# Kernel optimization log

Measured on AMD Instinct MI355X. Metric: run time of the kernel, lower is better.

The kernel has to match this reference:

```python
import jax, jax.numpy as jnp
import numpy as np

B, H, W, D = 1, 256, 256, 256
HEADS, DH = 8, 64
INNER = HEADS * DH


def setup_inputs() -> dict:
    key = jax.random.key(0)
    ks = jax.random.split(key, 6)
    s = 0.02  # init scale for weights
    return {
        "x": jax.random.normal(ks[0], (B, H, W, D), jnp.float32),
        "edges": jax.random.normal(ks[1], (B, H, H, D), jnp.float32),
        "mask": jnp.ones((B, H, W), jnp.bool_),
        "ln_g": jnp.ones((D,), jnp.float32),
        "ln_b": jnp.zeros((D,), jnp.float32),
        "Wq": jax.random.normal(ks[2], (D, INNER), jnp.float32) * s,
        "Wkv": jax.random.normal(ks[3], (D, 2 * INNER), jnp.float32) * s,
        "Wo": jax.random.normal(ks[4], (INNER, D), jnp.float32) * s,
        "bo": jnp.zeros((D,), jnp.float32),
        "Wg": jnp.zeros((D, INNER), jnp.float32),  # gating weight init 0
        "bg": jnp.ones((INNER,), jnp.float32),     # gating bias init 1
        "We": jax.random.normal(ks[5], (D, HEADS), jnp.float32) * s,
    }


def reference(x, edges, mask, ln_g, ln_b, Wq, Wkv, Wo, bo, Wg, bg, We):
    b, h, w, d = x.shape
    heads = We.shape[1]
    inner = Wq.shape[1]
    dh = inner // heads
    scale = dh ** -0.5

    # LayerNorm over last dim (eps=1e-5)
    mu = jnp.mean(x, axis=-1, keepdims=True)
    var = jnp.mean((x - mu) ** 2, axis=-1, keepdims=True)
    xn = (x - mu) * jax.lax.rsqrt(var + 1e-5) * ln_g + ln_b

    # pair bias from edges: (b, heads, i, j) with i=j=h
    bias = jnp.einsum('bijd,dh->bhij', edges, We)

    # row attention: tokens along h, batch over (b, w)
    xw = jnp.transpose(xn, (0, 2, 1, 3))              # (b, w, h, d)
    q = (xw @ Wq).reshape(b, w, h, heads, dh)
    kv = (xw @ Wkv).reshape(b, w, h, 2, heads, dh)
    k, v = kv[..., 0, :, :], kv[..., 1, :, :]

    # (b, w, heads, i, j)
    dots = jnp.einsum('bwihd,bwjhd->bwhij', q, k) * scale
    dots = dots + bias[:, None]                       # broadcast over w

    m = jnp.transpose(mask, (0, 2, 1))                # (b, w, h)
    pair_mask = m[:, :, None, :, None] & m[:, :, None, None, :]
    dots = jnp.where(pair_mask, dots, -jnp.finfo(dots.dtype).max)

    attn = jax.nn.softmax(dots, axis=-1)
    out = jnp.einsum('bwhij,bwjhd->bwihd', attn, v).reshape(b, w, h, inner)

    gates = xw @ Wg + bg
    out = (out * gates) @ Wo + bo                     # (b, w, h, d)
    out = jnp.transpose(out, (0, 2, 1, 3))            # (b, h, w, d)
    return out  # axial_attn_count == 1
```

## Files before the change

kernel.cpp:

```cpp
#include <hip/hip_runtime.h>
#include <hip/hip_bf16.h>
#include <stdint.h>

#define Hh     256
#define Ww     256
#define Dd     256
#define NHEADS 8
#define DH     64
#define INNER  512

typedef __attribute__((ext_vector_type(8))) short  bf16x8;
typedef __attribute__((ext_vector_type(4))) float  f32x4;

__device__ __forceinline__ unsigned short f2bfu(float f){
  __hip_bfloat16 h = __float2bfloat16(f);
  return *reinterpret_cast<unsigned short*>(&h);
}
__device__ __forceinline__ float bfu2f(unsigned short u){
  union { uint32_t i; float f; } a; a.i = ((uint32_t)u) << 16; return a.f;
}

__device__ __forceinline__ void async_cp16(unsigned short* lds_base_uniform,
                                           const unsigned short* g){
  __builtin_amdgcn_global_load_lds(
      (const __attribute__((address_space(1))) void*)g,
      (__attribute__((address_space(3))) void*)lds_base_uniform,
      16, 0, 0);
}

__global__ __launch_bounds__(256) void ln_kernel(const float* __restrict__ x,
        const float* __restrict__ lng, const float* __restrict__ lnb,
        unsigned short* __restrict__ xnb){
  int wv = threadIdx.x >> 6, l = threadIdx.x & 63;
  int row = blockIdx.x * 4 + wv;
  int h = row >> 8, w = row & 255;
  float4 v = *(const float4*)(x + (size_t)row * Dd + l * 4);
  float s1 = v.x + v.y + v.z + v.w;
  float s2 = v.x*v.x + v.y*v.y + v.z*v.z + v.w*v.w;
  #pragma unroll
  for (int off = 32; off; off >>= 1){
    s1 += __shfl_xor(s1, off, 64);
    s2 += __shfl_xor(s2, off, 64);
  }
  float mu  = s1 * (1.0f/256.0f);
  float var = s2 * (1.0f/256.0f) - mu*mu;
  float rs  = rsqrtf(var + 1e-5f);
  float4 g = *(const float4*)(lng + l*4);
  float4 b = *(const float4*)(lnb + l*4);
  union { unsigned short u[4]; uint2 v2; } pk;
  pk.u[0] = f2bfu((v.x - mu)*rs*g.x + b.x);
  pk.u[1] = f2bfu((v.y - mu)*rs*g.y + b.y);
  pk.u[2] = f2bfu((v.z - mu)*rs*g.z + b.z);
  pk.u[3] = f2bfu((v.w - mu)*rs*g.w + b.w);
  *(uint2*)(xnb + ((size_t)w * Hh + h) * Dd + l * 4) = pk.v2;
}

__global__ __launch_bounds__(256) void bias_kernel(const float* __restrict__ edges,
        const float* __restrict__ We, float* __restrict__ bias){
  const int t = threadIdx.x, wv = t >> 6, l = t & 63;
  float Wr[4][8];
  #pragma unroll
  for (int q = 0; q < 4; q++){
    float4 w0 = *(const float4*)(We + (l*4 + q) * 8);
    float4 w1 = *(const float4*)(We + (l*4 + q) * 8 + 4);
    Wr[q][0]=w0.x; Wr[q][1]=w0.y; Wr[q][2]=w0.z; Wr[q][3]=w0.w;
    Wr[q][4]=w1.x; Wr[q][5]=w1.y; Wr[q][6]=w1.z; Wr[q][7]=w1.w;
  }
  const int base = (blockIdx.x * 4 + wv) * 16;
  for (int i = 0; i < 16; i += 2){
    float4 eA = *(const float4*)(edges + (size_t)(base + i)     * 256 + l * 4);
    float4 eB = *(const float4*)(edges + (size_t)(base + i + 1) * 256 + l * 4);
    float aA[8], aB[8];
    #pragma unroll
    for (int h = 0; h < 8; h++){
      aA[h] = eA.x*Wr[0][h] + eA.y*Wr[1][h] + eA.z*Wr[2][h] + eA.w*Wr[3][h];
      aB[h] = eB.x*Wr[0][h] + eB.y*Wr[1][h] + eB.z*Wr[2][h] + eB.w*Wr[3][h];
    }
    #pragma unroll
    for (int h = 0; h < 8; h++){
      #pragma unroll
      for (int off = 1; off < 8; off <<= 1){
        aA[h] += __shfl_xor(aA[h], off, 64);
        aB[h] += __shfl_xor(aB[h], off, 64);
      }
    }
    float vA = (l&1) ? ((l&2) ? ((l&4)?aA[7]:aA[3]) : ((l&4)?aA[5]:aA[1]))
                     : ((l&2) ? ((l&4)?aA[6]:aA[2]) : ((l&4)?aA[4]:aA[0]));
    float vB = (l&1) ? ((l&2) ? ((l&4)?aB[7]:aB[3]) : ((l&4)?aB[5]:aB[1]))
                     : ((l&2) ? ((l&4)?aB[6]:aB[2]) : ((l&4)?aB[4]:aB[0]));
    #pragma unroll
    for (int off = 8; off < 64; off <<= 1){
      vA += __shfl_xor(vA, off, 64);
      vB += __shfl_xor(vB, off, 64);
    }
    if (l < 8)       bias[(size_t)l       * 65536 + base + i]     = vA;
    else if (l < 16) bias[(size_t)(l & 7) * 65536 + base + i + 1] = vB;
  }
}

__global__ __launch_bounds__(256) void transpose_w(const float* __restrict__ src,
        unsigned short* __restrict__ dst, int K, int N){
  __shared__ float ts[32][33];
  int n0 = blockIdx.x * 32, k0 = blockIdx.y * 32;
  int tx = threadIdx.x & 31, ty = threadIdx.x >> 5;
  #pragma unroll
  for (int i = 0; i < 32; i += 8)
    ts[ty + i][tx] = src[(size_t)(k0 + ty + i) * N + n0 + tx];
  __syncthreads();
  #pragma unroll
  for (int i = 0; i < 32; i += 8)
    dst[(size_t)(n0 + ty + i) * K + k0 + tx] = f2bfu(ts[tx][ty + i]);
}

__global__ __launch_bounds__(512, 2) void fused_qkvg_attn(
        const unsigned short* __restrict__ xnb,
        const unsigned short* __restrict__ WtA,
        const float* __restrict__ bias_all,
        const float* __restrict__ bg,
        unsigned short* __restrict__ ao){
  __shared__ unsigned short smem[68096];
  unsigned short* Sst = smem;
  unsigned short* Kl  = smem + 32768;
  unsigned short* Vl  = smem + 51200;
  const int t    = threadIdx.x;
  const int bid  = blockIdx.x;
  const int w    = bid & 255, head = bid >> 8;
  const int lane = t & 63, wv = t >> 6;
  const int lm   = lane & 15, quad = lane >> 4;
  const int row4 = t >> 2;
  const int cc   = (t & 3) ^ ((t >> 3) & 3);
  const int wvb  = wv * 512;
  const int xr   = (quad ^ ((lm >> 1) & 3)) * 8;

  const unsigned short* gA0 = xnb + ((size_t)(w * 256 + row4)) * 256 + cc * 8;
  const unsigned short* gA1 = gA0 + 128 * 256;
  const int nB0 = row4, nB1 = row4 + 128;
  const unsigned short* gB0 = WtA + ((size_t)((nB0 >> 6) * 512 + head * 64 + (nB0 & 63))) * 256 + cc * 8;
  const unsigned short* gB1 = WtA + ((size_t)((nB1 >> 6) * 512 + head * 64 + (nB1 & 63))) * 256 + cc * 8;

  f32x4 acc[2][16];
  #pragma unroll
  for (int s = 0; s < 2; s++)
    #pragma unroll
    for (int nt = 0; nt < 16; nt++) acc[s][nt] = (f32x4){0.f,0.f,0.f,0.f};

  {
    async_cp16(Sst + wvb,               gA0);
    async_cp16(Sst + 4096 + wvb,        gA1);
    async_cp16(Sst + 8192 + wvb,        gB0);
    async_cp16(Sst + 12288 + wvb,       gB1);
  }
  __syncthreads();
  for (int step = 0; step < 8; step++){
    const int cur = step & 1;
    if (step < 7){
      const int k0 = (step + 1) * 32;
      async_cp16(Sst + (cur^1)*16384 + wvb,         gA0 + k0);
      async_cp16(Sst + (cur^1)*16384 + 4096 + wvb,  gA1 + k0);
      async_cp16(Sst + (cur^1)*16384 + 8192 + wvb,  gB0 + k0);
      async_cp16(Sst + (cur^1)*16384 + 12288 + wvb, gB1 + k0);
    }
    bf16x8 a0 = *(const bf16x8*)&Sst[cur*16384 + (wv*32      + lm) * 32 + xr];
    bf16x8 a1 = *(const bf16x8*)&Sst[cur*16384 + (wv*32 + 16 + lm) * 32 + xr];
    #pragma unroll
    for (int h8 = 0; h8 < 2; h8++){
      bf16x8 b[8];
      #pragma unroll
      for (int i = 0; i < 8; i++)
        b[i] = *(const bf16x8*)&Sst[cur*16384 + 8192 + ((h8*8 + i)*16 + lm) * 32 + xr];
      #pragma unroll
      for (int i = 0; i < 8; i++){
        acc[0][h8*8+i] = __builtin_amdgcn_mfma_f32_16x16x32_bf16(a0, b[i], acc[0][h8*8+i], 0, 0, 0);
        acc[1][h8*8+i] = __builtin_amdgcn_mfma_f32_16x16x32_bf16(a1, b[i], acc[1][h8*8+i], 0, 0, 0);
      }
    }
    __syncthreads();
  }

  #pragma unroll
  for (int s = 0; s < 2; s++){
    #pragma unroll
    for (int nt = 4; nt < 8; nt++){
      int d = (nt - 4) * 16 + lm;
      #pragma unroll
      for (int r = 0; r < 4; r++){
        int key = wv*32 + s*16 + quad*4 + r;
        Kl[key * 72 + d] = f2bfu(acc[s][nt][r]);
      }
    }
    #pragma unroll
    for (int nt = 8; nt < 12; nt++){
      int d  = (nt - 8) * 16 + lm;
      int j0 = wv*32 + s*16 + quad*4;
      union { unsigned short u[4]; uint2 v2; } pk;
      #pragma unroll
      for (int r = 0; r < 4; r++) pk.u[r] = f2bfu(acc[s][nt][r]);
      *(uint2*)&Vl[d * 264 + j0] = pk.v2;
    }
  }
  __syncthreads();

  unsigned short* Qb = Sst + wv * 4096;
  unsigned short* Pb = Qb + 1152;
  const float* bias_h = bias_all + (size_t)head * 65536;
  float bgv[4];
  #pragma unroll
  for (int nt = 0; nt < 4; nt++) bgv[nt] = bg[head * 64 + nt*16 + lm];

  #pragma unroll
  for (int qt = 0; qt < 2; qt++){
    const int qb = wv*32 + qt*16;
    #pragma unroll
    for (int nt = 0; nt < 4; nt++)
      #pragma unroll
      for (int r = 0; r < 4; r++)
        Qb[(quad*4 + r) * 72 + nt*16 + lm] = f2bfu(acc[qt][nt][r]);
    f32x4 s2[16];
    #pragma unroll
    for (int nt2 = 0; nt2 < 16; nt2++) s2[nt2] = (f32x4){0.f,0.f,0.f,0.f};
    #pragma unroll
    for (int c = 0; c < 2; c++){
      bf16x8 qf = *(const bf16x8*)&Qb[lm * 72 + c*32 + quad*8];
      #pragma unroll
      for (int nt2 = 0; nt2 < 16; nt2++){
        bf16x8 kf = *(const bf16x8*)&Kl[(nt2*16 + lm) * 72 + c*32 + quad*8];
        s2[nt2] = __builtin_amdgcn_mfma_f32_16x16x32_bf16(qf, kf, s2[nt2], 0, 0, 0);
      }
    }
    float mx[4] = {-3.0e38f, -3.0e38f, -3.0e38f, -3.0e38f};
    #pragma unroll
    for (int nt2 = 0; nt2 < 16; nt2++)
      #pragma unroll
      for (int r = 0; r < 4; r++){
        float b = bias_h[(size_t)(qb + quad*4 + r) * 256 + nt2*16 + lm];
        s2[nt2][r] = s2[nt2][r] * 0.125f + b;
        mx[r] = fmaxf(mx[r], s2[nt2][r]);
      }
    #pragma unroll
    for (int r = 0; r < 4; r++){
      #pragma unroll
      for (int off = 1; off < 16; off <<= 1) mx[r] = fmaxf(mx[r], __shfl_xor(mx[r], off, 64));
    }
    float sum[4] = {0.f, 0.f, 0.f, 0.f};
    #pragma unroll
    for (int nt2 = 0; nt2 < 16; nt2++)
      #pragma unroll
      for (int r = 0; r < 4; r++){
        s2[nt2][r] = __expf(s2[nt2][r] - mx[r]);
        sum[r] += s2[nt2][r];
      }
    #pragma unroll
    for (int r = 0; r < 4; r++){
      #pragma unroll
      for (int off = 1; off < 16; off <<= 1) sum[r] += __shfl_xor(sum[r], off, 64);
      sum[r] = 1.0f / sum[r];
    }
    f32x4 o[4];
    #pragma unroll
    for (int nt = 0; nt < 4; nt++) o[nt] = (f32x4){0.f,0.f,0.f,0.f};
    #pragma unroll
    for (int kh = 0; kh < 2; kh++){
      #pragma unroll
      for (int nt2 = 0; nt2 < 8; nt2++)
        #pragma unroll
        for (int r = 0; r < 4; r++)
          Pb[(quad*4 + r) * 136 + nt2*16 + lm] = f2bfu(s2[kh*8 + nt2][r] * sum[r]);
      #pragma unroll
      for (int c2 = 0; c2 < 4; c2++){
        bf16x8 pf = *(const bf16x8*)&Pb[lm * 136 + c2*32 + quad*8];
        #pragma unroll
        for (int nt = 0; nt < 4; nt++){
          bf16x8 vf = *(const bf16x8*)&Vl[(nt*16 + lm) * 264 + kh*128 + c2*32 + quad*8];
          o[nt] = __builtin_amdgcn_mfma_f32_16x16x32_bf16(pf, vf, o[nt], 0, 0, 0);
        }
      }
    }
    #pragma unroll
    for (int nt = 0; nt < 4; nt++)
      #pragma unroll
      for (int r = 0; r < 4; r++){
        float g = acc[qt][12 + nt][r] + bgv[nt];
        Qb[(quad*4 + r) * 72 + nt*16 + lm] = f2bfu(o[nt][r] * g);
      }
    int rr = lane >> 2, d0 = (lane & 3) * 16;
    bf16x8 o0 = *(const bf16x8*)&Qb[rr * 72 + d0];
    bf16x8 o1 = *(const bf16x8*)&Qb[rr * 72 + d0 + 8];
    size_t tok = (size_t)(w * 256 + qb + rr);
    *(bf16x8*)(ao + tok * INNER + head * DH + d0)     = o0;
    *(bf16x8*)(ao + tok * INNER + head * DH + d0 + 8) = o1;
  }
}

__global__ __launch_bounds__(256) void gemm_proj_tiled(
        const unsigned short* __restrict__ ao,
        const unsigned short* __restrict__ WtO,
        const float* __restrict__ bo,
        float* __restrict__ out){
  __shared__ unsigned short lds[2][10240];
  const int t    = threadIdx.x;
  const int m0   = blockIdx.x * 64;
  const int lane = t & 63, wv = t >> 6;
  const int lm   = lane & 15, quad = lane >> 4;
  const int row4 = t >> 2;
  const int cc   = (t & 3) ^ ((t >> 3) & 3);
  const int wvb  = wv * 512;
  const unsigned short* gA = ao + (size_t)(m0 + row4) * INNER + cc * 8;
  const unsigned short* gB[4];
  #pragma unroll
  for (int i = 0; i < 4; i++)
    gB[i] = WtO + (size_t)(i * 64 + row4) * INNER + cc * 8;
  const int xr = (quad ^ ((lm >> 1) & 3)) * 8;

  f32x4 acc[4][4];
  #pragma unroll
  for (int mt = 0; mt < 4; mt++)
    #pragma unroll
    for (int nt = 0; nt < 4; nt++) acc[mt][nt] = (f32x4){0.f,0.f,0.f,0.f};

  async_cp16(&lds[0][wvb], gA);
  #pragma unroll
  for (int i = 0; i < 4; i++)
    async_cp16(&lds[0][2048 + i * 2048 + wvb], gB[i]);
  __syncthreads();

  for (int step = 0; step < 16; step++){
    const int cur = step & 1;
    if (step < 15){
      const int k0 = (step + 1) * 32;
      async_cp16(&lds[cur ^ 1][wvb], gA + k0);
      #pragma unroll
      for (int i = 0; i < 4; i++)
        async_cp16(&lds[cur ^ 1][2048 + i * 2048 + wvb], gB[i] + k0);
    }
    bf16x8 a[4], b[4];
    #pragma unroll
    for (int mt = 0; mt < 4; mt++)
      a[mt] = *(const bf16x8*)&lds[cur][(mt * 16 + lm) * 32 + xr];
    #pragma unroll
    for (int nt = 0; nt < 4; nt++)
      b[nt] = *(const bf16x8*)&lds[cur][2048 + (wv * 64 + nt * 16 + lm) * 32 + xr];
    #pragma unroll
    for (int mt = 0; mt < 4; mt++)
      #pragma unroll
      for (int nt = 0; nt < 4; nt++)
        acc[mt][nt] = __builtin_amdgcn_mfma_f32_16x16x32_bf16(a[mt], b[nt], acc[mt][nt], 0, 0, 0);
    __syncthreads();
  }

  #pragma unroll
  for (int mt = 0; mt < 4; mt++)
    #pragma unroll
    for (int nt = 0; nt < 4; nt++){
      int col = wv * 64 + nt * 16 + lm;
      float bb = bo[col];
      #pragma unroll
      for (int r = 0; r < 4; r++){
        int row = m0 + mt * 16 + quad * 4 + r;
        int h = row & 255, ww = row >> 8;
        out[((size_t)h * Ww + ww) * Dd + col] = acc[mt][nt][r] + bb;
      }
    }
}

extern "C" void kernel_launch(void* const* d_in, const int* in_sizes, int n_in,
                              void* d_out, int out_size, void* d_ws, size_t ws_size,
                              hipStream_t stream){
  const float* x     = (const float*)d_in[0];
  const float* edges = (const float*)d_in[1];
  const float* ln_g  = (const float*)d_in[3];
  const float* ln_b  = (const float*)d_in[4];
  const float* Wq    = (const float*)d_in[5];
  const float* Wkv   = (const float*)d_in[6];
  const float* Wo    = (const float*)d_in[7];
  const float* bo    = (const float*)d_in[8];
  const float* Wg    = (const float*)d_in[9];
  const float* bg    = (const float*)d_in[10];
  const float* We    = (const float*)d_in[11];
  float* out = (float*)d_out;

  char* ws = (char*)d_ws;
  unsigned short* ao  = (unsigned short*)(ws + 33554432);
  unsigned short* WtO = (unsigned short*)(ws + 100663296);
  char* dob = (char*)d_out;
  unsigned short* xnb  = (unsigned short*)dob;
  float*          bias = (float*)(dob + 33554432);
  unsigned short* WtA  = (unsigned short*)(dob + 35651584);

  ln_kernel  <<<16384, 256, 0, stream>>>(x, ln_g, ln_b, xnb);
  bias_kernel<<< 1024, 256, 0, stream>>>(edges, We, bias);
  transpose_w<<<dim3(16,  8), 256, 0, stream>>>(Wq,  WtA,                     Dd, 512);
  transpose_w<<<dim3(32,  8), 256, 0, stream>>>(Wkv, WtA + (size_t)512*Dd,    Dd, 1024);
  transpose_w<<<dim3(16,  8), 256, 0, stream>>>(Wg,  WtA + (size_t)1536*Dd,   Dd, 512);
  transpose_w<<<dim3( 8, 16), 256, 0, stream>>>(Wo,  WtO,                     INNER, 256);
  fused_qkvg_attn<<<2048, 512, 0, stream>>>(xnb, WtA, bias, bg, ao);
  gemm_proj_tiled<<<1024, 256, 0, stream>>>(ao, WtO, bo, out);
}
```

Baseline: 461.8 us.

## Swizzle LDS layouts and transpose MFMA operands for vectorized Q/K/V/P stores

Swaps MFMA operand order for the Q and K projection tiles so each lane holds four consecutive columns, which allows packed 8-byte LDS stores. Padded LDS strides are replaced with XOR-swizzled layouts to avoid bank conflicts. The two query sub-tiles are processed together so each K/V fragment load feeds two MFMAs, and bias loads become float4 reads. Holding more accumulators live raises register pressure, which could cost occupancy or cause spills.

```diff
diff --git a/kernel.cpp b/kernel.cpp
--- a/kernel.cpp
+++ b/kernel.cpp
@@ -18,6 +18,11 @@
 }
 __device__ __forceinline__ float bfu2f(unsigned short u){
   union { uint32_t i; float f; } a; a.i = ((uint32_t)u) << 16; return a.f;
+}
+__device__ __forceinline__ uint2 pk4(f32x4 v){
+  union { unsigned short u[4]; uint2 d; } p;
+  p.u[0] = f2bfu(v[0]); p.u[1] = f2bfu(v[1]); p.u[2] = f2bfu(v[2]); p.u[3] = f2bfu(v[3]);
+  return p.d;
 }
 
 __device__ __forceinline__ void async_cp16(unsigned short* lds_base_uniform,
@@ -118,19 +123,19 @@
         const float* __restrict__ bias_all,
         const float* __restrict__ bg,
         unsigned short* __restrict__ ao){
-  __shared__ unsigned short smem[68096];
+  __shared__ unsigned short smem[65536];
   unsigned short* Sst = smem;
   unsigned short* Kl  = smem + 32768;
-  unsigned short* Vl  = smem + 51200;
+  unsigned short* Vl  = smem + 49152;
   const int t    = threadIdx.x;
-  const int bid  = blockIdx.x;
-  const int w    = bid & 255, head = bid >> 8;
+  const int w    = blockIdx.x & 255, head = blockIdx.x >> 8;
   const int lane = t & 63, wv = t >> 6;
   const int lm   = lane & 15, quad = lane >> 4;
   const int row4 = t >> 2;
   const int cc   = (t & 3) ^ ((t >> 3) & 3);
   const int wvb  = wv * 512;
   const int xr   = (quad ^ ((lm >> 1) & 3)) * 8;
+  const int sw8  = (lm & 7) << 3;
 
   const unsigned short* gA0 = xnb + ((size_t)(w * 256 + row4)) * 256 + cc * 8;
   const unsigned short* gA1 = gA0 + 128 * 256;
@@ -144,12 +149,10 @@
     #pragma unroll
     for (int nt = 0; nt < 16; nt++) acc[s][nt] = (f32x4){0.f,0.f,0.f,0.f};
 
-  {
-    async_cp16(Sst + wvb,               gA0);
-    async_cp16(Sst + 4096 + wvb,        gA1);
-    async_cp16(Sst + 8192 + wvb,        gB0);
-    async_cp16(Sst + 12288 + wvb,       gB1);
-  }
+  async_cp16(Sst + wvb,          gA0);
+  async_cp16(Sst + 4096 + wvb,   gA1);
+  async_cp16(Sst + 8192 + wvb,   gB0);
+  async_cp16(Sst + 12288 + wvb,  gB1);
   __syncthreads();
   for (int step = 0; step < 8; step++){
     const int cur = step & 1;
@@ -162,132 +165,144 @@
     }
     bf16x8 a0 = *(const bf16x8*)&Sst[cur*16384 + (wv*32      + lm) * 32 + xr];
     bf16x8 a1 = *(const bf16x8*)&Sst[cur*16384 + (wv*32 + 16 + lm) * 32 + xr];
-    #pragma unroll
-    for (int h8 = 0; h8 < 2; h8++){
+    {
       bf16x8 b[8];
       #pragma unroll
       for (int i = 0; i < 8; i++)
-        b[i] = *(const bf16x8*)&Sst[cur*16384 + 8192 + ((h8*8 + i)*16 + lm) * 32 + xr];
+        b[i] = *(const bf16x8*)&Sst[cur*16384 + 8192 + (i*16 + lm) * 32 + xr];
       #pragma unroll
       for (int i = 0; i < 8; i++){
-        acc[0][h8*8+i] = __builtin_amdgcn_mfma_f32_16x16x32_bf16(a0, b[i], acc[0][h8*8+i], 0, 0, 0);
-        acc[1][h8*8+i] = __builtin_amdgcn_mfma_f32_16x16x32_bf16(a1, b[i], acc[1][h8*8+i], 0, 0, 0);
+        acc[0][i] = __builtin_amdgcn_mfma_f32_16x16x32_bf16(b[i], a0, acc[0][i], 0, 0, 0);
+        acc[1][i] = __builtin_amdgcn_mfma_f32_16x16x32_bf16(b[i], a1, acc[1][i], 0, 0, 0);
+      }
+    }
+    {
+      bf16x8 b[8];
+      #pragma unroll
+      for (int i = 0; i < 8; i++)
+        b[i] = *(const bf16x8*)&Sst[cur*16384 + 8192 + ((8+i)*16 + lm) * 32 + xr];
+      #pragma unroll
+      for (int i = 0; i < 8; i++){
+        acc[0][8+i] = __builtin_amdgcn_mfma_f32_16x16x32_bf16(a0, b[i], acc[0][8+i], 0, 0, 0);
+        acc[1][8+i] = __builtin_amdgcn_mfma_f32_16x16x32_bf16(a1, b[i], acc[1][8+i], 0, 0, 0);
       }
     }
     __syncthreads();
   }
 
+  unsigned short* slot = Sst + wv * 4096;
   #pragma unroll
   for (int s = 0; s < 2; s++){
-    #pragma unroll
-    for (int nt = 4; nt < 8; nt++){
-      int d = (nt - 4) * 16 + lm;
-      #pragma unroll
-      for (int r = 0; r < 4; r++){
-        int key = wv*32 + s*16 + quad*4 + r;
-        Kl[key * 72 + d] = f2bfu(acc[s][nt][r]);
-      }
-    }
-    #pragma unroll
-    for (int nt = 8; nt < 12; nt++){
-      int d  = (nt - 8) * 16 + lm;
-      int j0 = wv*32 + s*16 + quad*4;
-      union { unsigned short u[4]; uint2 v2; } pk;
-      #pragma unroll
-      for (int r = 0; r < 4; r++) pk.u[r] = f2bfu(acc[s][nt][r]);
-      *(uint2*)&Vl[d * 264 + j0] = pk.v2;
+    const int tok = wv*32 + s*16 + lm;
+    #pragma unroll
+    for (int i = 0; i < 4; i++)
+      *(uint2*)&slot[(s*16 + lm)*64 + ((i*16 + quad*4) ^ sw8)] = pk4(acc[s][i]);
+    #pragma unroll
+    for (int i = 4; i < 8; i++)
+      *(uint2*)&Kl[tok*64 + (((i-4)*16 + quad*4) ^ sw8)] = pk4(acc[s][i]);
+    #pragma unroll
+    for (int i = 8; i < 12; i++){
+      int d = (i-8)*16 + lm;
+      *(uint2*)&Vl[d*256 + ((wv*32 + s*16 + quad*4) ^ ((d&7) << 3))] = pk4(acc[s][i]);
     }
   }
   __syncthreads();
 
-  unsigned short* Qb = Sst + wv * 4096;
-  unsigned short* Pb = Qb + 1152;
   const float* bias_h = bias_all + (size_t)head * 65536;
   float bgv[4];
   #pragma unroll
   for (int nt = 0; nt < 4; nt++) bgv[nt] = bg[head * 64 + nt*16 + lm];
 
+  f32x4 s2[2][16];
+  #pragma unroll
+  for (int qt = 0; qt < 2; qt++)
+    #pragma unroll
+    for (int nt2 = 0; nt2 < 16; nt2++) s2[qt][nt2] = (f32x4){0.f,0.f,0.f,0.f};
+  #pragma unroll
+  for (int c = 0; c < 2; c++){
+    bf16x8 qf0 = *(const bf16x8*)&slot[(     lm)*64 + ((c*32 + quad*8) ^ sw8)];
+    bf16x8 qf1 = *(const bf16x8*)&slot[(16 + lm)*64 + ((c*32 + quad*8) ^ sw8)];
+    #pragma unroll
+    for (int nt2 = 0; nt2 < 16; nt2++){
+      bf16x8 kf = *(const bf16x8*)&Kl[(nt2*16 + lm)*64 + ((c*32 + quad*8) ^ sw8)];
+      s2[0][nt2] = __builtin_amdgcn_mfma_f32_16x16x32_bf16(kf, qf0, s2[0][nt2], 0, 0, 0);
+      s2[1][nt2] = __builtin_amdgcn_mfma_f32_16x16x32_bf16(kf, qf1, s2[1][nt2], 0, 0, 0);
+    }
+  }
+  float rs[2];
   #pragma unroll
   for (int qt = 0; qt < 2; qt++){
-    const int qb = wv*32 + qt*16;
-    #pragma unroll
-    for (int nt = 0; nt < 4; nt++)
-      #pragma unroll
-      for (int r = 0; r < 4; r++)
-        Qb[(quad*4 + r) * 72 + nt*16 + lm] = f2bfu(acc[qt][nt][r]);
-    f32x4 s2[16];
-    #pragma unroll
-    for (int nt2 = 0; nt2 < 16; nt2++) s2[nt2] = (f32x4){0.f,0.f,0.f,0.f};
-    #pragma unroll
-    for (int c = 0; c < 2; c++){
-      bf16x8 qf = *(const bf16x8*)&Qb[lm * 72 + c*32 + quad*8];
-      #pragma unroll
-      for (int nt2 = 0; nt2 < 16; nt2++){
-        bf16x8 kf = *(const bf16x8*)&Kl[(nt2*16 + lm) * 72 + c*32 + quad*8];
-        s2[nt2] = __builtin_amdgcn_mfma_f32_16x16x32_bf16(qf, kf, s2[nt2], 0, 0, 0);
-      }
-    }
-    float mx[4] = {-3.0e38f, -3.0e38f, -3.0e38f, -3.0e38f};
+    float m = -3.0e38f;
+    #pragma unroll
+    for (int nt2 = 0; nt2 < 16; nt2++){
+      float4 b4 = *(const float4*)(bias_h + (size_t)(wv*32 + qt*16 + lm) * 256 + nt2*16 + quad*4);
+      s2[qt][nt2][0] = s2[qt][nt2][0]*0.125f + b4.x;
+      s2[qt][nt2][1] = s2[qt][nt2][1]*0.125f + b4.y;
+      s2[qt][nt2][2] = s2[qt][nt2][2]*0.125f + b4.z;
+      s2[qt][nt2][3] = s2[qt][nt2][3]*0.125f + b4.w;
+      m = fmaxf(m, fmaxf(fmaxf(s2[qt][nt2][0], s2[qt][nt2][1]),
+                         fmaxf(s2[qt][nt2][2], s2[qt][nt2][3])));
+    }
+    m = fmaxf(m, __shfl_xor(m, 16, 64));
+    m = fmaxf(m, __shfl_xor(m, 32, 64));
+    float sm = 0.f;
     #pragma unroll
     for (int nt2 = 0; nt2 < 16; nt2++)
       #pragma unroll
       for (int r = 0; r < 4; r++){
-        float b = bias_h[(size_t)(qb + quad*4 + r) * 256 + nt2*16 + lm];
-        s2[nt2][r] = s2[nt2][r] * 0.125f + b;
-        mx[r] = fmaxf(mx[r], s2[nt2][r]);
-      }
-    #pragma unroll
-    for (int r = 0; r < 4; r++){
-      #pragma unroll
-      for (int off = 1; off < 16; off <<= 1) mx[r] = fmaxf(mx[r], __shfl_xor(mx[r], off, 64));
-    }
-    float sum[4] = {0.f, 0.f, 0.f, 0.f};
-    #pragma unroll
-    for (int nt2 = 0; nt2 < 16; nt2++)
-      #pragma unroll
-      for (int r = 0; r < 4; r++){
-        s2[nt2][r] = __expf(s2[nt2][r] - mx[r]);
-        sum[r] += s2[nt2][r];
-      }
-    #pragma unroll
-    for (int r = 0; r < 4; r++){
-      #pragma unroll
-      for (int off = 1; off < 16; off <<= 1) sum[r] += __shfl_xor(sum[r], off, 64);
-      sum[r] = 1.0f / sum[r];
-    }
-    f32x4 o[4];
-    #pragma unroll
-    for (int nt = 0; nt < 4; nt++) o[nt] = (f32x4){0.f,0.f,0.f,0.f};
-    #pragma unroll
-    for (int kh = 0; kh < 2; kh++){
-      #pragma unroll
-      for (int nt2 = 0; nt2 < 8; nt2++)
+        s2[qt][nt2][r] = __expf(s2[qt][nt2][r] - m);
+        sm += s2[qt][nt2][r];
+      }
+    sm += __shfl_xor(sm, 16, 64);
+    sm += __shfl_xor(sm, 32, 64);
+    rs[qt] = 1.0f / sm;
+  }
+  f32x4 o[2][4];
+  #pragma unroll
+  for (int qt = 0; qt < 2; qt++)
+    #pragma unroll
+    for (int nt = 0; nt < 4; nt++) o[qt][nt] = (f32x4){0.f,0.f,0.f,0.f};
+  #pragma unroll
+  for (int kh = 0; kh < 2; kh++){
+    #pragma unroll
+    for (int qt = 0; qt < 2; qt++)
+      #pragma unroll
+      for (int n8 = 0; n8 < 8; n8++){
+        f32x4 p;
         #pragma unroll
-        for (int r = 0; r < 4; r++)
-          Pb[(quad*4 + r) * 136 + nt2*16 + lm] = f2bfu(s2[kh*8 + nt2][r] * sum[r]);
-      #pragma unroll
-      for (int c2 = 0; c2 < 4; c2++){
-        bf16x8 pf = *(const bf16x8*)&Pb[lm * 136 + c2*32 + quad*8];
-        #pragma unroll
-        for (int nt = 0; nt < 4; nt++){
-          bf16x8 vf = *(const bf16x8*)&Vl[(nt*16 + lm) * 264 + kh*128 + c2*32 + quad*8];
-          o[nt] = __builtin_amdgcn_mfma_f32_16x16x32_bf16(pf, vf, o[nt], 0, 0, 0);
-        }
-      }
-    }
+        for (int r = 0; r < 4; r++) p[r] = s2[qt][kh*8 + n8][r] * rs[qt];
+        *(uint2*)&slot[qt*2048 + lm*128 + ((n8*16 + quad*4) ^ sw8)] = pk4(p);
+      }
+    #pragma unroll
+    for (int c2 = 0; c2 < 4; c2++){
+      bf16x8 pf0 = *(const bf16x8*)&slot[       lm*128 + ((c2*32 + quad*8) ^ sw8)];
+      bf16x8 pf1 = *(const bf16x8*)&slot[2048 + lm*128 + ((c2*32 + quad*8) ^ sw8)];
+      #pragma unroll
+      for (int nt = 0; nt < 4; nt++){
+        bf16x8 vf = *(const bf16x8*)&Vl[(nt*16 + lm)*256 + ((kh*128 + c2*32 + quad*8) ^ sw8)];
+        o[0][nt] = __builtin_amdgcn_mfma_f32_16x16x32_bf16(pf0, vf, o[0][nt], 0, 0, 0);
+        o[1][nt] = __builtin_amdgcn_mfma_f32_16x16x32_bf16(pf1, vf, o[1][nt], 0, 0, 0);
+      }
+    }
+  }
+  #pragma unroll
+  for (int qt = 0; qt < 2; qt++)
     #pragma unroll
     for (int nt = 0; nt < 4; nt++)
       #pragma unroll
       for (int r = 0; r < 4; r++){
         float g = acc[qt][12 + nt][r] + bgv[nt];
-        Qb[(quad*4 + r) * 72 + nt*16 + lm] = f2bfu(o[nt][r] * g);
-      }
-    int rr = lane >> 2, d0 = (lane & 3) * 16;
-    bf16x8 o0 = *(const bf16x8*)&Qb[rr * 72 + d0];
-    bf16x8 o1 = *(const bf16x8*)&Qb[rr * 72 + d0 + 8];
-    size_t tok = (size_t)(w * 256 + qb + rr);
-    *(bf16x8*)(ao + tok * INNER + head * DH + d0)     = o0;
-    *(bf16x8*)(ao + tok * INNER + head * DH + d0 + 8) = o1;
+        int q = qt*16 + quad*4 + r;
+        slot[q*64 + ((nt*16 + lm) ^ ((q&7) << 3))] = f2bfu(o[qt][nt][r] * g);
+      }
+  {
+    int rr = lane >> 1, dh = (lane & 1) * 32;
+    size_t tb = (size_t)(w*256 + wv*32 + rr) * INNER + head * DH + dh;
+    #pragma unroll
+    for (int j = 0; j < 4; j++){
+      bf16x8 ov = *(const bf16x8*)&slot[rr*64 + ((dh + j*8) ^ ((rr&7) << 3))];
+      *(bf16x8*)(ao + tb + j*8) = ov;
+    }
   }
 }
 
```

Measured after the change: 420.5 us. -8.9%, faster.
